# Performance work log

Hardware: AMD Instinct MI355X
Metric: run time of the kernel (lower is better)

## Reference

```python
import jax, jax.numpy as jnp
import numpy as np

BN_EPS = 1e-5


def setup_inputs() -> dict:
    key = jax.random.key(0)
    ks = jax.random.split(key, 4)
    N, V, C = 64, 512, 512
    K, OUT = 2, 512
    x = jax.random.normal(ks[0], (N, V, C), dtype=jnp.float32)
    A = jax.random.uniform(ks[1], (N, K, V, V), dtype=jnp.float32) / V
    conv_w = jax.random.normal(ks[2], (2 * OUT, C), dtype=jnp.float32) / np.sqrt(C)
    conv_b = jax.random.normal(ks[3], (2 * OUT,), dtype=jnp.float32) * 0.01
    gamma = jnp.ones((2 * OUT,), dtype=jnp.float32)
    beta = jnp.zeros((2 * OUT,), dtype=jnp.float32)
    eps_p = jnp.zeros((1,), dtype=jnp.float32)
    return {"x": x, "A": A, "conv_w": conv_w, "conv_b": conv_b,
            "gamma": gamma, "beta": beta, "eps_p": eps_p}


def reference(x, A, conv_w, conv_b, gamma, beta, eps_p):
    # x: (N, V, C); A: (N, K, V, V)
    N, V, C = x.shape
    K = A.shape[1]
    # 1x1 Conv1d over nodes: (N, 2*out, V)
    h = jnp.einsum('nvc,oc->nov', x, conv_w) + conv_b[None, :, None]
    # BatchNorm1d, training-mode batch stats (biased variance, per channel)
    mean = jnp.mean(h, axis=(0, 2), keepdims=True)
    var = jnp.var(h, axis=(0, 2), keepdims=True)
    h = (h - mean) * jax.lax.rsqrt(var + BN_EPS) * gamma[None, :, None] + beta[None, :, None]
    c2 = h.shape[1]
    h = h.reshape(N, K, c2 // K, V)  # (N, K, out, V)
    # graph propagation: x A then (x A) A^T, contracted over node dims
    t = jnp.einsum('nkcm,nkme->nkce', h, A)
    At = jnp.transpose(A, (0, 1, 3, 2))
    y = jnp.einsum('nkce,nkem->ncm', t, At)  # (N, out, V)
    out = (1.0 + eps_p[0]) * x + jnp.transpose(y, (0, 2, 1))
    return out, At
```

## Files before the change

kernel.cpp:

```cpp
#include <hip/hip_runtime.h>
#include <stdint.h>

typedef __bf16 bf16x8 __attribute__((ext_vector_type(8)));
typedef float f32x4 __attribute__((ext_vector_type(4)));
typedef unsigned short us4_t __attribute__((ext_vector_type(4)));
typedef unsigned short us8_t __attribute__((ext_vector_type(8)));

#define LDSK 40

__device__ __forceinline__ unsigned short f2bf(float f) {
  __bf16 b = (__bf16)f;
  return __builtin_bit_cast(unsigned short, b);
}
__device__ __forceinline__ float bf2f(unsigned short u) {
  union { uint32_t u; float f; } v; v.u = ((uint32_t)u) << 16;
  return v.f;
}

__device__ __forceinline__ void gload16(const void* g, void* l) {
  __builtin_amdgcn_global_load_lds(
      (const __attribute__((address_space(1))) void*)g,
      (__attribute__((address_space(3))) void*)l, 16, 0, 0);
}

__device__ __forceinline__ void stage_tile(const unsigned short* g, size_t ldg,
                                           unsigned short* lds, int wid, int lane) {
#pragma unroll
  for (int i = 0; i < 2; ++i) {
    int seg = wid * 2 + i;
    const unsigned short* gp = g + (size_t)(seg * 16 + (lane >> 2)) * ldg + (lane & 3) * 8;
    gload16(gp, lds + seg * 512);
  }
}

__device__ __forceinline__ void stage_tile_f32(const float* g, size_t ldg,
                                               float* lds, int wid, int lane) {
#pragma unroll
  for (int i = 0; i < 4; ++i) {
    int seg = wid * 4 + i;
    int r = seg * 8 + (lane >> 3);
    int gsw = (lane & 7) ^ (r & 7);
    const float* gp = g + (size_t)r * ldg + gsw * 4;
    gload16(gp, lds + seg * 256);
  }
}

__device__ __forceinline__ bf16x8 fragf(const float* lds, int row, int lk) {
  const float* rp = lds + row * 32;
  const int m = row & 7;
  f32x4 q0 = *(const f32x4*)(rp + ((((lk * 2) ^ m)) << 2));
  f32x4 q1 = *(const f32x4*)(rp + ((((lk * 2 + 1) ^ m)) << 2));
  bf16x8 r;
  r[0] = (__bf16)q0[0]; r[1] = (__bf16)q0[1]; r[2] = (__bf16)q0[2]; r[3] = (__bf16)q0[3];
  r[4] = (__bf16)q1[0]; r[5] = (__bf16)q1[1]; r[6] = (__bf16)q1[2]; r[7] = (__bf16)q1[3];
  return r;
}

__global__ __launch_bounds__(256) void k_convert(
    const float* __restrict__ X, const float* __restrict__ W,
    unsigned short* __restrict__ Xb, unsigned short* __restrict__ Wb) {
  const size_t idx = (size_t)blockIdx.x * 256 + threadIdx.x;
  const size_t stride = (size_t)gridDim.x * 256;
  for (size_t i = idx; i < (size_t)16777216 / 8; i += stride) {
    float4 f0 = ((const float4*)X)[2 * i], f1 = ((const float4*)X)[2 * i + 1];
    us8_t w = { f2bf(f0.x), f2bf(f0.y), f2bf(f0.z), f2bf(f0.w),
                f2bf(f1.x), f2bf(f1.y), f2bf(f1.z), f2bf(f1.w) };
    ((us8_t*)Xb)[i] = w;
  }
  for (size_t i = idx; i < (size_t)524288 / 8; i += stride) {
    float4 f0 = ((const float4*)W)[2 * i], f1 = ((const float4*)W)[2 * i + 1];
    us8_t w = { f2bf(f0.x), f2bf(f0.y), f2bf(f0.z), f2bf(f0.w),
                f2bf(f1.x), f2bf(f1.y), f2bf(f1.z), f2bf(f1.w) };
    ((us8_t*)Wb)[i] = w;
  }
}

__global__ __launch_bounds__(256) void k_gemm1(
    const unsigned short* __restrict__ Wb, const unsigned short* __restrict__ Xb,
    const float* __restrict__ convb, unsigned short* __restrict__ H) {
  __shared__ unsigned short As[128][32];
  __shared__ unsigned short Bs[128][32];
  const int tid = threadIdx.x;
  const int L = blockIdx.x;
  const int xcd = L & 7, slot = L >> 3;
  const int n = xcd * 8 + (slot >> 5);
  const int tile = slot & 31;
  const int tm = tile >> 2, tn = tile & 3;
  const unsigned short* gA = Wb + (size_t)tm * 128 * 512;
  const unsigned short* gB = Xb + ((size_t)n * 512 + tn * 128) * 512;
  const int lane = tid & 63, wid = tid >> 6;
  const int wr = (wid >> 1) * 64, wc = (wid & 1) * 64;
  const int lr = lane & 15, lk = lane >> 4;
  f32x4 acc[4][4] = {};
  for (int k0 = 0; k0 < 512; k0 += 32) {
    stage_tile(gA + k0, 512, &As[0][0], wid, lane);
    stage_tile(gB + k0, 512, &Bs[0][0], wid, lane);
    __syncthreads();
    bf16x8 a[4], b[4];
#pragma unroll
    for (int mi = 0; mi < 4; ++mi) a[mi] = *(const bf16x8*)&As[wr + mi * 16 + lr][lk * 8];
#pragma unroll
    for (int ni = 0; ni < 4; ++ni) b[ni] = *(const bf16x8*)&Bs[wc + ni * 16 + lr][lk * 8];
#pragma unroll
    for (int mi = 0; mi < 4; ++mi)
#pragma unroll
      for (int ni = 0; ni < 4; ++ni)
        acc[mi][ni] = __builtin_amdgcn_mfma_f32_16x16x32_bf16(a[mi], b[ni], acc[mi][ni], 0, 0, 0);
    __syncthreads();
  }
  unsigned short* Hn = H + (size_t)n * 1024 * 512;
#pragma unroll
  for (int mi = 0; mi < 4; ++mi)
#pragma unroll
    for (int i = 0; i < 4; ++i) {
      int o = tm * 128 + wr + mi * 16 + lk * 4 + i;
      float bias = convb[o];
#pragma unroll
      for (int ni = 0; ni < 4; ++ni) {
        int v = tn * 128 + wc + ni * 16 + lr;
        Hn[(size_t)o * 512 + v] = f2bf(acc[mi][ni][i] + bias);
      }
    }
}

__global__ __launch_bounds__(256) void k_bn(
    const unsigned short* __restrict__ H, const float* __restrict__ gamma,
    const float* __restrict__ beta, float* __restrict__ sc_sh) {
  const int o = blockIdx.x;
  const int tid = threadIdx.x;
  const int g = tid >> 6, l = tid & 63;
  float s1 = 0.f, s2 = 0.f;
  for (int step = 0; step < 16; ++step) {
    int n = g + step * 4;
    const us8_t* row = (const us8_t*)(H + ((size_t)n * 1024 + o) * 512);
    us8_t v = row[l];
#pragma unroll
    for (int j = 0; j < 8; ++j) { float f = bf2f(v[j]); s1 += f; s2 += f * f; }
  }
  __shared__ float r1[256], r2[256];
  r1[tid] = s1; r2[tid] = s2;
  __syncthreads();
  for (int off = 128; off > 0; off >>= 1) {
    if (tid < off) { r1[tid] += r1[tid + off]; r2[tid] += r2[tid + off]; }
    __syncthreads();
  }
  if (tid == 0) {
    float mean = r1[0] * (1.0f / 32768.0f);
    float var = r2[0] * (1.0f / 32768.0f) - mean * mean;
    float s = gamma[o] * rsqrtf(var + 1e-5f);
    sc_sh[o] = s;
    sc_sh[1024 + o] = beta[o] - mean * s;
  }
}

__global__ __launch_bounds__(256) void k_affine(
    unsigned short* __restrict__ H, const float* __restrict__ sc_sh) {
  const size_t idx = (size_t)blockIdx.x * 256 + threadIdx.x;
  const size_t stride = (size_t)gridDim.x * 256;
  const size_t total8 = (size_t)64 * 1024 * 512 / 8;
  for (size_t i = idx; i < total8; i += stride) {
    size_t base = i * 8;
    int o = (int)((base >> 9) & 1023);
    float sc = sc_sh[o], sh = sc_sh[1024 + o];
    us8_t v = ((const us8_t*)H)[i];
    us8_t w;
#pragma unroll
    for (int j = 0; j < 8; ++j) w[j] = f2bf(fmaf(bf2f(v[j]), sc, sh));
    ((us8_t*)H)[i] = w;
  }
}

__global__ __launch_bounds__(256) void k_aat(
    const float* __restrict__ A, unsigned short* __restrict__ B2) {
  __shared__ __align__(16) float Afs[128 * 32];
  __shared__ __align__(16) float Bfs[128 * 32];
  const int tid = threadIdx.x;
  const int L = blockIdx.x;
  const int xcd = L & 7, slot = L >> 3;
  const int nk = xcd * 16 + (slot >> 4);
  const int tile = slot & 15;
  const int tm = tile >> 2, tn = tile & 3;
  const float* Ank = A + (size_t)nk * 262144;
  const float* gA = Ank + (size_t)tm * 128 * 512;
  const float* gB = Ank + (size_t)tn * 128 * 512;
  const int lane = tid & 63, wid = tid >> 6;
  const int wr = (wid >> 1) * 64, wc = (wid & 1) * 64;
  const int lr = lane & 15, lk = lane >> 4;
  f32x4 acc[4][4] = {};
  for (int k0 = 0; k0 < 512; k0 += 32) {
    stage_tile_f32(gA + k0, 512, Afs, wid, lane);
    stage_tile_f32(gB + k0, 512, Bfs, wid, lane);
    __syncthreads();
    bf16x8 a[4], b[4];
#pragma unroll
    for (int mi = 0; mi < 4; ++mi) a[mi] = fragf(Afs, wr + mi * 16 + lr, lk);
#pragma unroll
    for (int ni = 0; ni < 4; ++ni) b[ni] = fragf(Bfs, wc + ni * 16 + lr, lk);
#pragma unroll
    for (int mi = 0; mi < 4; ++mi)
#pragma unroll
      for (int ni = 0; ni < 4; ++ni)
        acc[mi][ni] = __builtin_amdgcn_mfma_f32_16x16x32_bf16(a[mi], b[ni], acc[mi][ni], 0, 0, 0);
    __syncthreads();
  }
  unsigned short* Bn = B2 + (size_t)nk * 262144;
#pragma unroll
  for (int mi = 0; mi < 4; ++mi)
#pragma unroll
    for (int i = 0; i < 4; ++i) {
      int m = tm * 128 + wr + mi * 16 + lk * 4 + i;
#pragma unroll
      for (int ni = 0; ni < 4; ++ni) {
        int mp = tn * 128 + wc + ni * 16 + lr;
        Bn[(size_t)m * 512 + mp] = f2bf(acc[mi][ni][i]);
      }
    }
}

template <bool AFFINE>
__global__ __launch_bounds__(256) void k_gemm3(
    const unsigned short* __restrict__ B2, const unsigned short* __restrict__ H,
    const float* __restrict__ sc_sh, const float* __restrict__ X,
    const float* __restrict__ epsp, float* __restrict__ out) {
  __shared__ unsigned short As[128][32];
  __shared__ unsigned short Bs[128][LDSK];
  __shared__ float s_sc[2][128], s_sh[2][128];
  const int tid = threadIdx.x;
  const int L = blockIdx.x;
  const int xcd = L & 7, slot = L >> 3;
  const int n = xcd * 8 + (slot >> 4);
  const int tile = slot & 15;
  const int tm = tile >> 2, tn = tile & 3;
  const int lane = tid & 63, wid = tid >> 6;
  const int wr = (wid >> 1) * 64, wc = (wid & 1) * 64;
  const int lr = lane & 15, lk = lane >> 4;
  if (AFFINE) {
    if (tid < 256) {
      int kkq = tid >> 7, r = tid & 127;
      s_sc[kkq][r] = sc_sh[kkq * 512 + tn * 128 + r];
      s_sh[kkq][r] = sc_sh[1024 + kkq * 512 + tn * 128 + r];
    }
    __syncthreads();
  }
  f32x4 acc[4][4] = {};
  for (int kk = 0; kk < 2; ++kk) {
    const unsigned short* gA = B2 + ((size_t)(n * 2 + kk) * 512 + tm * 128) * 512;
    const unsigned short* gB = H + ((size_t)n * 1024 + kk * 512 + tn * 128) * 512;
    for (int k0 = 0; k0 < 512; k0 += 32) {
      stage_tile(gA + k0, 512, &As[0][0], wid, lane);
#pragma unroll
      for (int i = 0; i < 2; ++i) {
        int s = tid + i * 256;
        int r = s >> 2, c8 = (s & 3) * 8;
        us8_t v = *(const us8_t*)(gB + (size_t)r * 512 + k0 + c8);
        if (AFFINE) {
          float sc = s_sc[kk][r], sh = s_sh[kk][r];
          us8_t w;
#pragma unroll
          for (int j = 0; j < 8; ++j) w[j] = f2bf(fmaf(bf2f(v[j]), sc, sh));
          *(us8_t*)&Bs[r][c8] = w;
        } else {
          *(us8_t*)&Bs[r][c8] = v;
        }
      }
      __syncthreads();
      bf16x8 a[4], b[4];
#pragma unroll
      for (int mi = 0; mi < 4; ++mi) a[mi] = *(const bf16x8*)&As[wr + mi * 16 + lr][lk * 8];
#pragma unroll
      for (int ni = 0; ni < 4; ++ni) b[ni] = *(const bf16x8*)&Bs[wc + ni * 16 + lr][lk * 8];
#pragma unroll
      for (int mi = 0; mi < 4; ++mi)
#pragma unroll
        for (int ni = 0; ni < 4; ++ni)
          acc[mi][ni] = __builtin_amdgcn_mfma_f32_16x16x32_bf16(a[mi], b[ni], acc[mi][ni], 0, 0, 0);
      __syncthreads();
    }
  }
  const float e1 = 1.0f + epsp[0];
#pragma unroll
  for (int mi = 0; mi < 4; ++mi)
#pragma unroll
    for (int i = 0; i < 4; ++i) {
      int v = tm * 128 + wr + mi * 16 + lk * 4 + i;
#pragma unroll
      for (int ni = 0; ni < 4; ++ni) {
        int c = tn * 128 + wc + ni * 16 + lr;
        size_t idx = ((size_t)n * 512 + v) * 512 + c;
        out[idx] = fmaf(e1, X[idx], acc[mi][ni][i]);
      }
    }
}

__global__ __launch_bounds__(256) void k_at(
    const float* __restrict__ A, float* __restrict__ At) {
  __shared__ float tile[64][65];
  const int nk = blockIdx.z;
  const int e0 = blockIdx.x * 64, m0 = blockIdx.y * 64;
  const float* src = A + (size_t)nk * 262144;
  float* dst = At + (size_t)nk * 262144;
  const int t = threadIdx.x;
#pragma unroll
  for (int j = 0; j < 4; ++j) {
    int ch = t + j * 256;
    int r = ch >> 4, c4 = (ch & 15) * 4;
    float4 f = *(const float4*)(src + (size_t)(m0 + r) * 512 + e0 + c4);
    tile[r][c4] = f.x; tile[r][c4 + 1] = f.y; tile[r][c4 + 2] = f.z; tile[r][c4 + 3] = f.w;
  }
  __syncthreads();
#pragma unroll
  for (int j = 0; j < 4; ++j) {
    int ch = t + j * 256;
    int e = ch >> 4, m4 = (ch & 15) * 4;
    float4 g = { tile[m4][e], tile[m4 + 1][e], tile[m4 + 2][e], tile[m4 + 3][e] };
    *(float4*)(dst + (size_t)(e0 + e) * 512 + m0 + m4) = g;
  }
}

extern "C" void kernel_launch(void* const* d_in, const int* in_sizes, int n_in,
                              void* d_out, int out_size, void* d_ws, size_t ws_size,
                              hipStream_t stream) {
  const float* x      = (const float*)d_in[0];
  const float* A      = (const float*)d_in[1];
  const float* conv_w = (const float*)d_in[2];
  const float* conv_b = (const float*)d_in[3];
  const float* gamma  = (const float*)d_in[4];
  const float* beta   = (const float*)d_in[5];
  const float* eps_p  = (const float*)d_in[6];

  float* out = (float*)d_out;
  float* At  = out + (size_t)16777216;

  unsigned short* B2 = (unsigned short*)At;
  unsigned short* H  = (unsigned short*)(At + (size_t)16777216);
  unsigned short* Xb = (unsigned short*)out;
  unsigned short* Wb = Xb + (size_t)16777216;

  const bool use_ws = (ws_size >= 8192);
  float* sc_sh = use_ws ? (float*)d_ws : out;

  k_convert<<<2048, 256, 0, stream>>>(x, conv_w, Xb, Wb);
  k_gemm1  <<<2048, 256, 0, stream>>>(Wb, Xb, conv_b, H);
  k_bn     <<<1024, 256, 0, stream>>>(H, gamma, beta, sc_sh);
  k_aat    <<<2048, 256, 0, stream>>>(A, B2);
  if (use_ws) {
    k_gemm3<true><<<1024, 256, 0, stream>>>(B2, H, sc_sh, x, eps_p, out);
  } else {
    k_affine<<<2048, 256, 0, stream>>>(H, sc_sh);
    k_gemm3<false><<<1024, 256, 0, stream>>>(B2, H, nullptr, x, eps_p, out);
  }
  k_at<<<dim3(8, 8, 128), 256, 0, stream>>>(A, At);
}
```

Before: 294.0 us.

## Fuse bf16 conversion and BatchNorm statistics into the first GEMM

```diff
diff --git a/kernel.cpp b/kernel.cpp
--- a/kernel.cpp
+++ b/kernel.cpp
@@ -56,51 +56,34 @@
   return r;
 }
 
-__global__ __launch_bounds__(256) void k_convert(
-    const float* __restrict__ X, const float* __restrict__ W,
-    unsigned short* __restrict__ Xb, unsigned short* __restrict__ Wb) {
-  const size_t idx = (size_t)blockIdx.x * 256 + threadIdx.x;
-  const size_t stride = (size_t)gridDim.x * 256;
-  for (size_t i = idx; i < (size_t)16777216 / 8; i += stride) {
-    float4 f0 = ((const float4*)X)[2 * i], f1 = ((const float4*)X)[2 * i + 1];
-    us8_t w = { f2bf(f0.x), f2bf(f0.y), f2bf(f0.z), f2bf(f0.w),
-                f2bf(f1.x), f2bf(f1.y), f2bf(f1.z), f2bf(f1.w) };
-    ((us8_t*)Xb)[i] = w;
-  }
-  for (size_t i = idx; i < (size_t)524288 / 8; i += stride) {
-    float4 f0 = ((const float4*)W)[2 * i], f1 = ((const float4*)W)[2 * i + 1];
-    us8_t w = { f2bf(f0.x), f2bf(f0.y), f2bf(f0.z), f2bf(f0.w),
-                f2bf(f1.x), f2bf(f1.y), f2bf(f1.z), f2bf(f1.w) };
-    ((us8_t*)Wb)[i] = w;
-  }
-}
-
+template <bool STATS>
 __global__ __launch_bounds__(256) void k_gemm1(
-    const unsigned short* __restrict__ Wb, const unsigned short* __restrict__ Xb,
-    const float* __restrict__ convb, unsigned short* __restrict__ H) {
-  __shared__ unsigned short As[128][32];
-  __shared__ unsigned short Bs[128][32];
+    const float* __restrict__ W, const float* __restrict__ X,
+    const float* __restrict__ convb, unsigned short* __restrict__ H,
+    float* __restrict__ psum, float* __restrict__ psq) {
+  __shared__ __align__(16) float Afs[128 * 32];
+  __shared__ __align__(16) float Bfs[128 * 32];
   const int tid = threadIdx.x;
   const int L = blockIdx.x;
   const int xcd = L & 7, slot = L >> 3;
   const int n = xcd * 8 + (slot >> 5);
   const int tile = slot & 31;
   const int tm = tile >> 2, tn = tile & 3;
-  const unsigned short* gA = Wb + (size_t)tm * 128 * 512;
-  const unsigned short* gB = Xb + ((size_t)n * 512 + tn * 128) * 512;
+  const float* gA = W + (size_t)tm * 128 * 512;
+  const float* gB = X + ((size_t)n * 512 + tn * 128) * 512;
   const int lane = tid & 63, wid = tid >> 6;
   const int wr = (wid >> 1) * 64, wc = (wid & 1) * 64;
   const int lr = lane & 15, lk = lane >> 4;
   f32x4 acc[4][4] = {};
   for (int k0 = 0; k0 < 512; k0 += 32) {
-    stage_tile(gA + k0, 512, &As[0][0], wid, lane);
-    stage_tile(gB + k0, 512, &Bs[0][0], wid, lane);
+    stage_tile_f32(gA + k0, 512, Afs, wid, lane);
+    stage_tile_f32(gB + k0, 512, Bfs, wid, lane);
     __syncthreads();
     bf16x8 a[4], b[4];
 #pragma unroll
-    for (int mi = 0; mi < 4; ++mi) a[mi] = *(const bf16x8*)&As[wr + mi * 16 + lr][lk * 8];
-#pragma unroll
-    for (int ni = 0; ni < 4; ++ni) b[ni] = *(const bf16x8*)&Bs[wc + ni * 16 + lr][lk * 8];
+    for (int mi = 0; mi < 4; ++mi) a[mi] = fragf(Afs, wr + mi * 16 + lr, lk);
+#pragma unroll
+    for (int ni = 0; ni < 4; ++ni) b[ni] = fragf(Bfs, wc + ni * 16 + lr, lk);
 #pragma unroll
     for (int mi = 0; mi < 4; ++mi)
 #pragma unroll
@@ -109,18 +92,83 @@
     __syncthreads();
   }
   unsigned short* Hn = H + (size_t)n * 1024 * 512;
+  float s1a[4][4], s2a[4][4];
 #pragma unroll
   for (int mi = 0; mi < 4; ++mi)
 #pragma unroll
     for (int i = 0; i < 4; ++i) {
       int o = tm * 128 + wr + mi * 16 + lk * 4 + i;
       float bias = convb[o];
+      float s1 = 0.f, s2 = 0.f;
 #pragma unroll
       for (int ni = 0; ni < 4; ++ni) {
         int v = tn * 128 + wc + ni * 16 + lr;
-        Hn[(size_t)o * 512 + v] = f2bf(acc[mi][ni][i] + bias);
+        float h = acc[mi][ni][i] + bias;
+        Hn[(size_t)o * 512 + v] = f2bf(h);
+        if (STATS) { s1 += h; s2 += h * h; }
       }
-    }
+      if (STATS) {
+#pragma unroll
+        for (int d = 1; d < 16; d <<= 1) {
+          s1 += __shfl_xor(s1, d);
+          s2 += __shfl_xor(s2, d);
+        }
+        s1a[mi][i] = s1; s2a[mi][i] = s2;
+      }
+    }
+  if (STATS) {
+    float* ps = Bfs;
+    __syncthreads();
+    if ((wid & 1) == 0 && (lane & 15) == 0) {
+#pragma unroll
+      for (int mi = 0; mi < 4; ++mi)
+#pragma unroll
+        for (int i = 0; i < 4; ++i) {
+          int cl = wr + mi * 16 + lk * 4 + i;
+          ps[cl] = s1a[mi][i]; ps[128 + cl] = s2a[mi][i];
+        }
+    }
+    __syncthreads();
+    if ((wid & 1) == 1 && (lane & 15) == 0) {
+#pragma unroll
+      for (int mi = 0; mi < 4; ++mi)
+#pragma unroll
+        for (int i = 0; i < 4; ++i) {
+          int cl = wr + mi * 16 + lk * 4 + i;
+          ps[cl] += s1a[mi][i]; ps[128 + cl] += s2a[mi][i];
+        }
+    }
+    __syncthreads();
+    if (tid < 128) {
+      int o = tm * 128 + tid;
+      int pc = n * 4 + tn;
+      psum[(size_t)o * 256 + pc] = ps[tid];
+      psq [(size_t)o * 256 + pc] = ps[128 + tid];
+    }
+  }
+}
+
+__global__ __launch_bounds__(256) void k_bn_final(
+    const float* __restrict__ psum, const float* __restrict__ psq,
+    const float* __restrict__ gamma, const float* __restrict__ beta,
+    float* __restrict__ sc_sh) {
+  const int o = blockIdx.x;
+  const int tid = threadIdx.x;
+  __shared__ float r1[256], r2[256];
+  r1[tid] = psum[(size_t)o * 256 + tid];
+  r2[tid] = psq[(size_t)o * 256 + tid];
+  __syncthreads();
+  for (int off = 128; off > 0; off >>= 1) {
+    if (tid < off) { r1[tid] += r1[tid + off]; r2[tid] += r2[tid + off]; }
+    __syncthreads();
+  }
+  if (tid == 0) {
+    float mean = r1[0] * (1.0f / 32768.0f);
+    float var = r2[0] * (1.0f / 32768.0f) - mean * mean;
+    float s = gamma[o] * rsqrtf(var + 1e-5f);
+    sc_sh[o] = s;
+    sc_sh[1024 + o] = beta[o] - mean * s;
+  }
 }
 
 __global__ __launch_bounds__(256) void k_bn(
@@ -333,20 +381,29 @@
 
   unsigned short* B2 = (unsigned short*)At;
   unsigned short* H  = (unsigned short*)(At + (size_t)16777216);
-  unsigned short* Xb = (unsigned short*)out;
-  unsigned short* Wb = Xb + (size_t)16777216;
-
-  const bool use_ws = (ws_size >= 8192);
-  float* sc_sh = use_ws ? (float*)d_ws : out;
-
-  k_convert<<<2048, 256, 0, stream>>>(x, conv_w, Xb, Wb);
-  k_gemm1  <<<2048, 256, 0, stream>>>(Wb, Xb, conv_b, H);
-  k_bn     <<<1024, 256, 0, stream>>>(H, gamma, beta, sc_sh);
-  k_aat    <<<2048, 256, 0, stream>>>(A, B2);
-  if (use_ws) {
+
+  const size_t WS_FAST = (size_t)(2048 + 2 * 262144) * sizeof(float);
+  float* wsf = (float*)d_ws;
+
+  if (ws_size >= WS_FAST) {
+    float* sc_sh = wsf;
+    float* psum  = wsf + 2048;
+    float* psq   = psum + 262144;
+    k_gemm1<true><<<2048, 256, 0, stream>>>(conv_w, x, conv_b, H, psum, psq);
+    k_bn_final   <<<1024, 256, 0, stream>>>(psum, psq, gamma, beta, sc_sh);
+    k_aat        <<<2048, 256, 0, stream>>>(A, B2);
     k_gemm3<true><<<1024, 256, 0, stream>>>(B2, H, sc_sh, x, eps_p, out);
+  } else if (ws_size >= 8192) {
+    float* sc_sh = wsf;
+    k_gemm1<false><<<2048, 256, 0, stream>>>(conv_w, x, conv_b, H, nullptr, nullptr);
+    k_bn          <<<1024, 256, 0, stream>>>(H, gamma, beta, sc_sh);
+    k_aat         <<<2048, 256, 0, stream>>>(A, B2);
+    k_gemm3<true> <<<1024, 256, 0, stream>>>(B2, H, sc_sh, x, eps_p, out);
   } else {
-    k_affine<<<2048, 256, 0, stream>>>(H, sc_sh);
+    float* sc_sh = out;
+    k_gemm1<false><<<2048, 256, 0, stream>>>(conv_w, x, conv_b, H, nullptr, nullptr);
+    k_bn          <<<1024, 256, 0, stream>>>(H, gamma, beta, sc_sh);
+    k_affine      <<<2048, 256, 0, stream>>>(H, sc_sh);
     k_gemm3<false><<<1024, 256, 0, stream>>>(B2, H, nullptr, x, eps_p, out);
   }
   k_at<<<dim3(8, 8, 128), 256, 0, stream>>>(A, At);
```

Result: slower. 313.5 us (+6.6%).

## Double-buffer LDS in GEMM kernels and pre-convert A to bf16

Applied to the files above, without the earlier changes.

```diff
diff --git a/kernel.cpp b/kernel.cpp
--- a/kernel.cpp
+++ b/kernel.cpp
@@ -3,10 +3,7 @@
 
 typedef __bf16 bf16x8 __attribute__((ext_vector_type(8)));
 typedef float f32x4 __attribute__((ext_vector_type(4)));
-typedef unsigned short us4_t __attribute__((ext_vector_type(4)));
 typedef unsigned short us8_t __attribute__((ext_vector_type(8)));
-
-#define LDSK 40
 
 __device__ __forceinline__ unsigned short f2bf(float f) {
   __bf16 b = (__bf16)f;
@@ -33,27 +30,21 @@
   }
 }
 
-__device__ __forceinline__ void stage_tile_f32(const float* g, size_t ldg,
-                                               float* lds, int wid, int lane) {
-#pragma unroll
-  for (int i = 0; i < 4; ++i) {
-    int seg = wid * 4 + i;
-    int r = seg * 8 + (lane >> 3);
-    int gsw = (lane & 7) ^ (r & 7);
-    const float* gp = g + (size_t)r * ldg + gsw * 4;
-    gload16(gp, lds + seg * 256);
-  }
-}
-
-__device__ __forceinline__ bf16x8 fragf(const float* lds, int row, int lk) {
-  const float* rp = lds + row * 32;
-  const int m = row & 7;
-  f32x4 q0 = *(const f32x4*)(rp + ((((lk * 2) ^ m)) << 2));
-  f32x4 q1 = *(const f32x4*)(rp + ((((lk * 2 + 1) ^ m)) << 2));
-  bf16x8 r;
-  r[0] = (__bf16)q0[0]; r[1] = (__bf16)q0[1]; r[2] = (__bf16)q0[2]; r[3] = (__bf16)q0[3];
-  r[4] = (__bf16)q1[0]; r[5] = (__bf16)q1[1]; r[6] = (__bf16)q1[2]; r[7] = (__bf16)q1[3];
-  return r;
+__device__ __forceinline__ void mfma_step(const unsigned short* As, const unsigned short* Bs,
+                                          int ldb, f32x4 (*acc)[4],
+                                          int wr, int wc, int lr, int lk) {
+  bf16x8 a[4], b[4];
+#pragma unroll
+  for (int mi = 0; mi < 4; ++mi)
+    a[mi] = *(const bf16x8*)(As + (wr + mi * 16 + lr) * 32 + lk * 8);
+#pragma unroll
+  for (int ni = 0; ni < 4; ++ni)
+    b[ni] = *(const bf16x8*)(Bs + (wc + ni * 16 + lr) * ldb + lk * 8);
+#pragma unroll
+  for (int mi = 0; mi < 4; ++mi)
+#pragma unroll
+    for (int ni = 0; ni < 4; ++ni)
+      acc[mi][ni] = __builtin_amdgcn_mfma_f32_16x16x32_bf16(a[mi], b[ni], acc[mi][ni], 0, 0, 0);
 }
 
 __global__ __launch_bounds__(256) void k_convert(
@@ -75,11 +66,22 @@
   }
 }
 
+__global__ __launch_bounds__(256) void k_convertA(
+    const float* __restrict__ A, unsigned short* __restrict__ Ab) {
+  const size_t idx = (size_t)blockIdx.x * 256 + threadIdx.x;
+  const size_t stride = (size_t)gridDim.x * 256;
+  for (size_t i = idx; i < (size_t)33554432 / 8; i += stride) {
+    float4 f0 = ((const float4*)A)[2 * i], f1 = ((const float4*)A)[2 * i + 1];
+    us8_t w = { f2bf(f0.x), f2bf(f0.y), f2bf(f0.z), f2bf(f0.w),
+                f2bf(f1.x), f2bf(f1.y), f2bf(f1.z), f2bf(f1.w) };
+    ((us8_t*)Ab)[i] = w;
+  }
+}
+
 __global__ __launch_bounds__(256) void k_gemm1(
     const unsigned short* __restrict__ Wb, const unsigned short* __restrict__ Xb,
     const float* __restrict__ convb, unsigned short* __restrict__ H) {
-  __shared__ unsigned short As[128][32];
-  __shared__ unsigned short Bs[128][32];
+  __shared__ unsigned short A0[4096], B0[4096], A1[4096], B1[4096];
   const int tid = threadIdx.x;
   const int L = blockIdx.x;
   const int xcd = L & 7, slot = L >> 3;
@@ -92,21 +94,19 @@
   const int wr = (wid >> 1) * 64, wc = (wid & 1) * 64;
   const int lr = lane & 15, lk = lane >> 4;
   f32x4 acc[4][4] = {};
-  for (int k0 = 0; k0 < 512; k0 += 32) {
-    stage_tile(gA + k0, 512, &As[0][0], wid, lane);
-    stage_tile(gB + k0, 512, &Bs[0][0], wid, lane);
-    __syncthreads();
-    bf16x8 a[4], b[4];
-#pragma unroll
-    for (int mi = 0; mi < 4; ++mi) a[mi] = *(const bf16x8*)&As[wr + mi * 16 + lr][lk * 8];
-#pragma unroll
-    for (int ni = 0; ni < 4; ++ni) b[ni] = *(const bf16x8*)&Bs[wc + ni * 16 + lr][lk * 8];
-#pragma unroll
-    for (int mi = 0; mi < 4; ++mi)
-#pragma unroll
-      for (int ni = 0; ni < 4; ++ni)
-        acc[mi][ni] = __builtin_amdgcn_mfma_f32_16x16x32_bf16(a[mi], b[ni], acc[mi][ni], 0, 0, 0);
-    __syncthreads();
+  stage_tile(gA, 512, A0, wid, lane);
+  stage_tile(gB, 512, B0, wid, lane);
+  for (int k0 = 0; k0 < 512; k0 += 64) {
+    __syncthreads();
+    stage_tile(gA + k0 + 32, 512, A1, wid, lane);
+    stage_tile(gB + k0 + 32, 512, B1, wid, lane);
+    mfma_step(A0, B0, 32, acc, wr, wc, lr, lk);
+    __syncthreads();
+    if (k0 + 64 < 512) {
+      stage_tile(gA + k0 + 64, 512, A0, wid, lane);
+      stage_tile(gB + k0 + 64, 512, B0, wid, lane);
+    }
+    mfma_step(A1, B1, 32, acc, wr, wc, lr, lk);
   }
   unsigned short* Hn = H + (size_t)n * 1024 * 512;
 #pragma unroll
@@ -171,37 +171,34 @@
 }
 
 __global__ __launch_bounds__(256) void k_aat(
-    const float* __restrict__ A, unsigned short* __restrict__ B2) {
-  __shared__ __align__(16) float Afs[128 * 32];
-  __shared__ __align__(16) float Bfs[128 * 32];
+    const unsigned short* __restrict__ Ab, unsigned short* __restrict__ B2) {
+  __shared__ unsigned short A0[4096], B0[4096], A1[4096], B1[4096];
   const int tid = threadIdx.x;
   const int L = blockIdx.x;
   const int xcd = L & 7, slot = L >> 3;
   const int nk = xcd * 16 + (slot >> 4);
   const int tile = slot & 15;
   const int tm = tile >> 2, tn = tile & 3;
-  const float* Ank = A + (size_t)nk * 262144;
-  const float* gA = Ank + (size_t)tm * 128 * 512;
-  const float* gB = Ank + (size_t)tn * 128 * 512;
+  const unsigned short* Ank = Ab + (size_t)nk * 262144;
+  const unsigned short* gA = Ank + (size_t)tm * 128 * 512;
+  const unsigned short* gB = Ank + (size_t)tn * 128 * 512;
   const int lane = tid & 63, wid = tid >> 6;
   const int wr = (wid >> 1) * 64, wc = (wid & 1) * 64;
   const int lr = lane & 15, lk = lane >> 4;
   f32x4 acc[4][4] = {};
-  for (int k0 = 0; k0 < 512; k0 += 32) {
-    stage_tile_f32(gA + k0, 512, Afs, wid, lane);
-    stage_tile_f32(gB + k0, 512, Bfs, wid, lane);
-    __syncthreads();
-    bf16x8 a[4], b[4];
-#pragma unroll
-    for (int mi = 0; mi < 4; ++mi) a[mi] = fragf(Afs, wr + mi * 16 + lr, lk);
-#pragma unroll
-    for (int ni = 0; ni < 4; ++ni) b[ni] = fragf(Bfs, wc + ni * 16 + lr, lk);
-#pragma unroll
-    for (int mi = 0; mi < 4; ++mi)
-#pragma unroll
-      for (int ni = 0; ni < 4; ++ni)
-        acc[mi][ni] = __builtin_amdgcn_mfma_f32_16x16x32_bf16(a[mi], b[ni], acc[mi][ni], 0, 0, 0);
-    __syncthreads();
+  stage_tile(gA, 512, A0, wid, lane);
+  stage_tile(gB, 512, B0, wid, lane);
+  for (int k0 = 0; k0 < 512; k0 += 64) {
+    __syncthreads();
+    stage_tile(gA + k0 + 32, 512, A1, wid, lane);
+    stage_tile(gB + k0 + 32, 512, B1, wid, lane);
+    mfma_step(A0, B0, 32, acc, wr, wc, lr, lk);
+    __syncthreads();
+    if (k0 + 64 < 512) {
+      stage_tile(gA + k0 + 64, 512, A0, wid, lane);
+      stage_tile(gB + k0 + 64, 512, B0, wid, lane);
+    }
+    mfma_step(A1, B1, 32, acc, wr, wc, lr, lk);
   }
   unsigned short* Bn = B2 + (size_t)nk * 262144;
 #pragma unroll
@@ -215,6 +212,31 @@
         Bn[(size_t)m * 512 + mp] = f2bf(acc[mi][ni][i]);
       }
     }
+}
+
+__device__ __forceinline__ void ldB(const unsigned short* gB, int k, int tid,
+                                    us8_t* va, us8_t* vb) {
+  int r0 = tid >> 2, c8 = (tid & 3) * 8;
+  *va = *(const us8_t*)(gB + (size_t)r0 * 512 + k + c8);
+  *vb = *(const us8_t*)(gB + (size_t)(r0 + 64) * 512 + k + c8);
+}
+
+template <bool AFFINE>
+__device__ __forceinline__ void wrB(unsigned short* Bs, us8_t va, us8_t vb,
+                                    float scA, float shA, float scB, float shB,
+                                    int tid) {
+  int r0 = tid >> 2, c8 = (tid & 3) * 8;
+  us8_t w;
+  if (AFFINE) {
+#pragma unroll
+    for (int j = 0; j < 8; ++j) w[j] = f2bf(fmaf(bf2f(va[j]), scA, shA));
+  } else w = va;
+  *(us8_t*)&Bs[r0 * 40 + c8] = w;
+  if (AFFINE) {
+#pragma unroll
+    for (int j = 0; j < 8; ++j) w[j] = f2bf(fmaf(bf2f(vb[j]), scB, shB));
+  } else w = vb;
+  *(us8_t*)&Bs[(r0 + 64) * 40 + c8] = w;
 }
 
 template <bool AFFINE>
@@ -222,9 +244,8 @@
     const unsigned short* __restrict__ B2, const unsigned short* __restrict__ H,
     const float* __restrict__ sc_sh, const float* __restrict__ X,
     const float* __restrict__ epsp, float* __restrict__ out) {
-  __shared__ unsigned short As[128][32];
-  __shared__ unsigned short Bs[128][LDSK];
-  __shared__ float s_sc[2][128], s_sh[2][128];
+  __shared__ unsigned short A0[4096], A1[4096];
+  __shared__ unsigned short Bs0[128 * 40], Bs1[128 * 40];
   const int tid = threadIdx.x;
   const int L = blockIdx.x;
   const int xcd = L & 7, slot = L >> 3;
@@ -234,47 +255,35 @@
   const int lane = tid & 63, wid = tid >> 6;
   const int wr = (wid >> 1) * 64, wc = (wid & 1) * 64;
   const int lr = lane & 15, lk = lane >> 4;
-  if (AFFINE) {
-    if (tid < 256) {
-      int kkq = tid >> 7, r = tid & 127;
-      s_sc[kkq][r] = sc_sh[kkq * 512 + tn * 128 + r];
-      s_sh[kkq][r] = sc_sh[1024 + kkq * 512 + tn * 128 + r];
-    }
-    __syncthreads();
-  }
   f32x4 acc[4][4] = {};
   for (int kk = 0; kk < 2; ++kk) {
     const unsigned short* gA = B2 + ((size_t)(n * 2 + kk) * 512 + tm * 128) * 512;
     const unsigned short* gB = H + ((size_t)n * 1024 + kk * 512 + tn * 128) * 512;
-    for (int k0 = 0; k0 < 512; k0 += 32) {
-      stage_tile(gA + k0, 512, &As[0][0], wid, lane);
-#pragma unroll
-      for (int i = 0; i < 2; ++i) {
-        int s = tid + i * 256;
-        int r = s >> 2, c8 = (s & 3) * 8;
-        us8_t v = *(const us8_t*)(gB + (size_t)r * 512 + k0 + c8);
-        if (AFFINE) {
-          float sc = s_sc[kk][r], sh = s_sh[kk][r];
-          us8_t w;
-#pragma unroll
-          for (int j = 0; j < 8; ++j) w[j] = f2bf(fmaf(bf2f(v[j]), sc, sh));
-          *(us8_t*)&Bs[r][c8] = w;
-        } else {
-          *(us8_t*)&Bs[r][c8] = v;
-        }
+    float scA = 0.f, shA = 0.f, scB = 0.f, shB = 0.f;
+    if (AFFINE) {
+      int r0 = tid >> 2;
+      int ch = kk * 512 + tn * 128;
+      scA = sc_sh[ch + r0];       shA = sc_sh[1024 + ch + r0];
+      scB = sc_sh[ch + r0 + 64];  shB = sc_sh[1024 + ch + r0 + 64];
+    }
+    us8_t va, vb;
+    ldB(gB, 0, tid, &va, &vb);
+    stage_tile(gA, 512, A0, wid, lane);
+    wrB<AFFINE>(Bs0, va, vb, scA, shA, scB, shB, tid);
+    for (int k0 = 0; k0 < 512; k0 += 64) {
+      __syncthreads();
+      stage_tile(gA + k0 + 32, 512, A1, wid, lane);
+      ldB(gB, k0 + 32, tid, &va, &vb);
+      mfma_step(A0, Bs0, 40, acc, wr, wc, lr, lk);
+      wrB<AFFINE>(Bs1, va, vb, scA, shA, scB, shB, tid);
+      __syncthreads();
+      const bool more = (k0 + 64 < 512);
+      if (more) {
+        stage_tile(gA + k0 + 64, 512, A0, wid, lane);
+        ldB(gB, k0 + 64, tid, &va, &vb);
       }
-      __syncthreads();
-      bf16x8 a[4], b[4];
-#pragma unroll
-      for (int mi = 0; mi < 4; ++mi) a[mi] = *(const bf16x8*)&As[wr + mi * 16 + lr][lk * 8];
-#pragma unroll
-      for (int ni = 0; ni < 4; ++ni) b[ni] = *(const bf16x8*)&Bs[wc + ni * 16 + lr][lk * 8];
-#pragma unroll
-      for (int mi = 0; mi < 4; ++mi)
-#pragma unroll
-        for (int ni = 0; ni < 4; ++ni)
-          acc[mi][ni] = __builtin_amdgcn_mfma_f32_16x16x32_bf16(a[mi], b[ni], acc[mi][ni], 0, 0, 0);
-      __syncthreads();
+      mfma_step(A1, Bs1, 40, acc, wr, wc, lr, lk);
+      if (more) wrB<AFFINE>(Bs0, va, vb, scA, shA, scB, shB, tid);
     }
   }
   const float e1 = 1.0f + epsp[0];
@@ -335,18 +344,26 @@
   unsigned short* H  = (unsigned short*)(At + (size_t)16777216);
   unsigned short* Xb = (unsigned short*)out;
   unsigned short* Wb = Xb + (size_t)16777216;
-
-  const bool use_ws = (ws_size >= 8192);
-  float* sc_sh = use_ws ? (float*)d_ws : out;
-
-  k_convert<<<2048, 256, 0, stream>>>(x, conv_w, Xb, Wb);
-  k_gemm1  <<<2048, 256, 0, stream>>>(Wb, Xb, conv_b, H);
-  k_bn     <<<1024, 256, 0, stream>>>(H, gamma, beta, sc_sh);
-  k_aat    <<<2048, 256, 0, stream>>>(A, B2);
-  if (use_ws) {
+  unsigned short* Ab = (unsigned short*)out;
+
+  float* wsf = (float*)d_ws;
+
+  if (ws_size >= 8192) {
+    float* sc_sh = wsf;
+    k_convert    <<<2048, 256, 0, stream>>>(x, conv_w, Xb, Wb);
+    k_gemm1      <<<2048, 256, 0, stream>>>(Wb, Xb, conv_b, H);
+    k_bn         <<<1024, 256, 0, stream>>>(H, gamma, beta, sc_sh);
+    k_convertA   <<<2048, 256, 0, stream>>>(A, Ab);
+    k_aat        <<<2048, 256, 0, stream>>>(Ab, B2);
     k_gemm3<true><<<1024, 256, 0, stream>>>(B2, H, sc_sh, x, eps_p, out);
   } else {
-    k_affine<<<2048, 256, 0, stream>>>(H, sc_sh);
+    float* sc_sh = out;
+    k_convert     <<<2048, 256, 0, stream>>>(x, conv_w, Xb, Wb);
+    k_gemm1       <<<2048, 256, 0, stream>>>(Wb, Xb, conv_b, H);
+    k_bn          <<<1024, 256, 0, stream>>>(H, gamma, beta, sc_sh);
+    k_affine      <<<2048, 256, 0, stream>>>(H, sc_sh);
+    k_convertA    <<<2048, 256, 0, stream>>>(A, Ab);
+    k_aat         <<<2048, 256, 0, stream>>>(Ab, B2);
     k_gemm3<false><<<1024, 256, 0, stream>>>(B2, H, nullptr, x, eps_p, out);
   }
   k_at<<<dim3(8, 8, 128), 256, 0, stream>>>(A, At);
```

New measurement: 324.3 us. +10.3%, slower.
